# Performance work log

Hardware: AMD Instinct MI355X
Metric: run time of the kernel (lower is better)

The kernel has to match this reference:

```python
import jax, jax.numpy as jnp
import numpy as np

B, C, H, W = 1, 256, 48, 64
HW = H * W
HIDDEN, CTX = 128, 64
LEVELS, RADIUS = 4, 4
WIN = 2 * RADIUS + 1
P = WIN * WIN                     # 81 lookup points per level
CORR_DIM = P * LEVELS             # 324
TOP_K = 3
ITERS = 4
STEP_ROT, STEP_TRANS = 0.02, 0.02


def _sample_templates():
    # 12 directions x 3 scales + identity = 37 pose perturbations (as in __init__)
    base = [([0,0,0],[1,0,0]),([0,0,0],[-1,0,0]),([0,0,0],[0,1,0]),([0,0,0],[0,-1,0]),
            ([0,0,0],[0,0,1]),([0,0,0],[0,0,-1]),([1,0,0],[0,0,0]),([-1,0,0],[0,0,0]),
            ([0,1,0],[0,0,0]),([0,-1,0],[0,0,0]),([0,0,1],[0,0,0]),([0,0,-1],[0,0,0])]
    scales = np.array([0.25, 1.0, 4.0], np.float32)
    rot = np.repeat(np.array([r for r, _ in base], np.float32), 3, axis=0)
    trs = np.repeat(np.array([t for _, t in base], np.float32), 3, axis=0)
    sc = np.tile(scales, 12)
    axes = rot / np.clip(np.linalg.norm(rot, axis=1, keepdims=True), 1e-8, None)
    ha = STEP_ROT * sc / 2.0
    dq = np.stack([np.cos(ha), axes[:, 0]*np.sin(ha), axes[:, 1]*np.sin(ha), axes[:, 2]*np.sin(ha)], -1)
    dt = trs * (STEP_TRANS * sc[:, None])
    dq = np.concatenate([dq, [[1., 0., 0., 0.]]], 0)
    dt = np.concatenate([dt, [[0., 0., 0.]]], 0)
    return jnp.asarray(dq), jnp.asarray(dt)

DQ, DT = _sample_templates()     # (37,4), (37,3)
N_SAMPLES = DQ.shape[0]


def qmul(q, r):
    w1, x1, y1, z1 = jnp.moveaxis(q, -1, 0)
    w2, x2, y2, z2 = jnp.moveaxis(r, -1, 0)
    return jnp.stack([w1*w2 - x1*x2 - y1*y2 - z1*z2,
                      w1*x2 + x1*w2 + y1*z2 - z1*y2,
                      w1*y2 - x1*z2 + y1*w2 + z1*x2,
                      w1*z2 + x1*y2 - y1*x2 + z1*w2], -1)


def qapply(q, v):
    qv = jnp.concatenate([jnp.zeros(v.shape[:-1] + (1,), v.dtype), v], -1)
    qc = q * jnp.array([1., -1., -1., -1.], q.dtype)
    return qmul(qmul(q, qv), qc)[..., 1:]


def quat_to_R(q):
    w, x, y, z = jnp.moveaxis(q, -1, 0)
    R = jnp.stack([1-2*(y*y+z*z), 2*(x*y-w*z), 2*(x*z+w*y),
                   2*(x*y+w*z), 1-2*(x*x+z*z), 2*(y*z-w*x),
                   2*(x*z-w*y), 2*(y*z+w*x), 1-2*(x*x+y*y)], -1)
    return R.reshape(q.shape[:-1] + (3, 3))


def conv3(x, w, b):
    y = jax.lax.conv_general_dilated(x, w, (1, 1), 'SAME',
                                     dimension_numbers=('NCHW', 'OIHW', 'NCHW'))
    return y + b[None, :, None, None]


def bilinear_lookup(corr_flat, Hl, Wl, x, y):
    # corr_flat: (B,HW,Hl*Wl); x,y: (B,N,HW,P) -> (B,N,HW,P), zero padding outside
    x0 = jnp.floor(x)
    y0 = jnp.floor(y)
    out = jnp.zeros(x.shape, corr_flat.dtype)
    def gather(idx):
        g = lambda ix: jnp.take_along_axis(corr_flat, ix, axis=-1)
        return jax.vmap(g, in_axes=1, out_axes=1)(idx)   # vmap over N, no corr copy
    for dx_, dy_ in ((0, 0), (1, 0), (0, 1), (1, 1)):
        xi = x0 + dx_
        yi = y0 + dy_
        wgt = (1 - jnp.abs(x - xi)) * (1 - jnp.abs(y - yi))
        valid = (xi >= 0) & (xi < Wl) & (yi >= 0) & (yi < Hl)
        idx = (jnp.clip(yi, 0, Hl - 1) * Wl + jnp.clip(xi, 0, Wl - 1)).astype(jnp.int32)
        out = out + jnp.where(valid, wgt, 0.0) * gather(idx)
    return out


def _forward(fmap_rgb, fmap_depth, depth, context, intrinsics,
             Wz, bz, Wr, br, Wq, bq, Wh, bh, Wfc, bfc):
    f32 = jnp.float32
    fx = 60. + 40. * intrinsics[:, 0]
    fy = 60. + 40. * intrinsics[:, 1]
    cx = W / 2. + 4. * (intrinsics[:, 2] - 0.5)
    cy = H / 2. + 4. * (intrinsics[:, 3] - 0.5)
    d = 4.0 + 20.0 * depth                                  # (B,H,W) metric depth

    # 4D correlation pyramid: corr[b,i,:,:] = <fmap_depth pixel i, fmap_rgb>
    fd = fmap_depth.reshape(B, C, HW).transpose(0, 2, 1)    # (B,HW,C)
    corr = jnp.einsum('bic,bchw->bihw', fd, fmap_rgb) / jnp.sqrt(f32(C))
    pyramid = []
    cl, Hl, Wl = corr, H, W
    for _ in range(LEVELS):
        pyramid.append((cl.reshape(B, HW, Hl * Wl), Hl, Wl))
        cl = cl.reshape(B, HW, Hl // 2, 2, Wl // 2, 2).mean(axis=(3, 5))
        Hl //= 2
        Wl //= 2

    # back-projected depth points (B,HW,3)
    vv, uu = jnp.meshgrid(jnp.arange(H, dtype=f32), jnp.arange(W, dtype=f32), indexing='ij')
    uu = uu.reshape(HW)
    vv = vv.reshape(HW)
    df = d.reshape(B, HW)
    X = jnp.stack([(uu[None] - cx[:, None]) / fx[:, None] * df,
                   (vv[None] - cy[:, None]) / fy[:, None] * df, df], -1)

    off = jnp.arange(-RADIUS, RADIUS + 1, dtype=f32)
    oy, ox = jnp.meshgrid(off, off, indexing='ij')
    ox = ox.reshape(P)
    oy = oy.reshape(P)

    pose = jnp.tile(jnp.array([1., 0., 0., 0., 0., 0., 0.], f32)[None, :], (B, 1))
    h = jnp.zeros((B, HIDDEN, H, W), f32)

    for _ in range(ITERS):
        qc, tc = pose[:, :4], pose[:, 4:7]
        quats = qmul(qc[:, None, :], DQ[None])              # (B,N,4)
        quats = quats / jnp.linalg.norm(quats, axis=-1, keepdims=True)
        trans = tc[:, None, :] + qapply(qc[:, None, :], DT[None])
        Rm = quat_to_R(quats)                               # (B,N,3,3)
        Xc = jnp.einsum('bnij,bpj->bnpi', Rm, X) + trans[:, :, None, :]
        z = jnp.clip(Xc[..., 2], 0.1, None)
        u = fx[:, None, None] * Xc[..., 0] / z + cx[:, None, None]   # (B,N,HW)
        v = fy[:, None, None] * Xc[..., 1] / z + cy[:, None, None]
        feats = []
        for lvl, (cfl, Hl_, Wl_) in enumerate(pyramid):
            s = f32(2 ** lvl)
            xl = u[..., None] / s + ox
            yl = v[..., None] / s + oy
            feats.append(bilinear_lookup(cfl, Hl_, Wl_, xl, yl))
        cf = jnp.concatenate(feats, -1)                     # (B,N,HW,CORR_DIM)
        conf = cf.mean(axis=(2, 3))                         # (B,N) sample confidence
        topv, topi = jax.lax.top_k(conf, TOP_K)
        wk = jax.nn.softmax(topv, axis=-1)                  # confidence-weighted top-K
        idx = jnp.broadcast_to(topi[:, :, None, None], (B, TOP_K, HW, CORR_DIM))
        sel = jnp.take_along_axis(cf, idx, axis=1)
        fused = (wk[:, :, None, None] * sel).sum(1)         # (B,HW,CORR_DIM)
        fused = fused.transpose(0, 2, 1).reshape(B, CORR_DIM, H, W)

        # ConvGRU update
        x_in = jnp.concatenate([fused, context], 1)
        hx = jnp.concatenate([h, x_in], 1)
        zg = jax.nn.sigmoid(conv3(hx, Wz, bz))
        rg = jax.nn.sigmoid(conv3(hx, Wr, br))
        qg = jnp.tanh(conv3(jnp.concatenate([rg * h, x_in], 1), Wq, bq))
        h = (1 - zg) * h + zg * qg

        # 7D pose delta head + quaternion/Lie-style update
        feat = jax.nn.relu(conv3(h, Wh, bh)).mean(axis=(2, 3))
        delta = 0.01 * (feat @ Wfc + bfc)                   # (B,7)
        dq = jnp.concatenate([1.0 + delta[:, :1], delta[:, 1:4]], -1)
        dq = dq / jnp.linalg.norm(dq, axis=-1, keepdims=True)
        tn = tc + qapply(qc, delta[:, 4:7])
        qn = qmul(qc, dq)
        qn = qn / jnp.linalg.norm(qn, axis=-1, keepdims=True)
        pose = jnp.concatenate([qn, tn], -1)
    return pose


def setup_inputs() -> dict:
    key = jax.random.key(0)
    ks = jax.random.split(key, 12)
    rn = lambda k, shape, s=1.0: s * jax.random.normal(k, shape, jnp.float32)
    Gin = HIDDEN + CORR_DIM + CTX
    sc = 1.0 / np.sqrt(Gin * 9)
    sh = 1.0 / np.sqrt(HIDDEN * 9)
    return {
        'fmap_rgb': rn(ks[0], (B, C, H, W)),
        'fmap_depth': rn(ks[1], (B, C, H, W)),
        'depth': jax.random.uniform(ks[2], (B, H, W), jnp.float32),
        'context': rn(ks[3], (B, CTX, H, W)),
        'intrinsics': jax.random.uniform(ks[4], (B, 4), jnp.float32),
        'Wz': rn(ks[5], (HIDDEN, Gin, 3, 3), sc), 'bz': jnp.zeros((HIDDEN,), jnp.float32),
        'Wr': rn(ks[6], (HIDDEN, Gin, 3, 3), sc), 'br': jnp.zeros((HIDDEN,), jnp.float32),
        'Wq': rn(ks[7], (HIDDEN, Gin, 3, 3), sc), 'bq': jnp.zeros((HIDDEN,), jnp.float32),
        'Wh': rn(ks[8], (HIDDEN, HIDDEN, 3, 3), sh), 'bh': jnp.zeros((HIDDEN,), jnp.float32),
        'Wfc': rn(ks[9], (HIDDEN, 7), 1.0 / np.sqrt(HIDDEN)), 'bfc': jnp.zeros((7,), jnp.float32),
    }


def reference(fmap_rgb, fmap_depth, depth, context, intrinsics,
              Wz, bz, Wr, br, Wq, bq, Wh, bh, Wfc, bfc):
    return _forward(fmap_rgb, fmap_depth, depth, context, intrinsics,
                    Wz, bz, Wr, br, Wq, bq, Wh, bh, Wfc, bfc)
```

## Files before the change

kernel.cpp:

```cpp
#include <hip/hip_runtime.h>
#include <math.h>

constexpr int kH = 48, kW = 64, kHW = 3072, kC = 256;
constexpr int kHidden = 128, kCtx = 64;
constexpr int kP = 81, kCorrDim = 324;
constexpr int kNS = 37, kIters = 4;
constexpr int kGin = kHidden + kCorrDim + kCtx;
constexpr int kCinPad = 544;
constexpr int kStepsBig = 17 * 9;
constexpr int kStepsH = 4 * 9;

constexpr int kSB0 = 0, kSB1 = 4292, kSB2 = 5720, kSB3 = 6292, kSBTot = 6580;
constexpr int kHB0 = 0, kHB1 = 3552, kHB2 = 4560, kHB3 = 4872, kHBTot = 4980;

constexpr size_t U_CORR0 = 0;
constexpr size_t U_CORR1 = U_CORR0 + (size_t)kHW * 3072;
constexpr size_t U_CORR2 = U_CORR1 + (size_t)kHW * 768;
constexpr size_t U_CORR3 = U_CORR2 + (size_t)kHW * 192;
constexpr size_t U_END0  = U_CORR3 + (size_t)kHW * 48;
constexpr size_t F_X     = U_END0 / 2;
constexpr size_t F_H     = F_X + (size_t)kHW * 3;
constexpr size_t F_ZPRE  = F_H + (size_t)kHidden * kHW;
constexpr size_t F_END1  = F_ZPRE + (size_t)kHidden * kHW;
constexpr size_t U_BUFT  = F_END1 * 2;
constexpr size_t U_RHT   = U_BUFT + (size_t)kHW * kCinPad;
constexpr size_t U_PZR   = U_RHT + (size_t)kHW * kHidden;
constexpr size_t U_PQ    = U_PZR + (size_t)kStepsBig * 256 * 32;
constexpr size_t U_PH    = U_PQ + (size_t)kStepsBig * 128 * 32;
constexpr size_t U_END2  = U_PH + (size_t)kStepsH * 128 * 32;
constexpr size_t F_BZR   = (U_END2 + 2) / 2;
constexpr size_t F_CONF  = F_BZR + 256;
constexpr size_t F_TK    = F_CONF + 64;
constexpr size_t F_POSE  = F_TK + 16;
constexpr size_t F_FEAT  = F_POSE + 16;
constexpr size_t F_END3  = F_FEAT + 128;
constexpr size_t U_FDT   = F_END3 * 2;
constexpr size_t U_QT    = U_FDT + (size_t)kHW * kC;
constexpr size_t U_SBOX  = U_FDT;

typedef __attribute__((ext_vector_type(8))) short short8;
typedef __attribute__((ext_vector_type(4))) float f32x4;

__device__ inline unsigned short f2b(float f) {
  unsigned int u = __float_as_uint(f);
  unsigned int r = u + 0x7FFF + ((u >> 16) & 1);
  return (unsigned short)(r >> 16);
}
__device__ inline float b2f(unsigned short u) {
  return __uint_as_float(((unsigned int)u) << 16);
}
__device__ inline int clampi(int v, int lo, int hi) { return min(max(v, lo), hi); }

__constant__ float c_rot[12][3] = {
  {0,0,0},{0,0,0},{0,0,0},{0,0,0},{0,0,0},{0,0,0},
  {1,0,0},{-1,0,0},{0,1,0},{0,-1,0},{0,0,1},{0,0,-1}};
__constant__ float c_trs[12][3] = {
  {1,0,0},{-1,0,0},{0,1,0},{0,-1,0},{0,0,1},{0,0,-1},
  {0,0,0},{0,0,0},{0,0,0},{0,0,0},{0,0,0},{0,0,0}};

__device__ inline void d_qmul(const float* q, const float* r, float* o) {
  o[0] = q[0]*r[0] - q[1]*r[1] - q[2]*r[2] - q[3]*r[3];
  o[1] = q[0]*r[1] + q[1]*r[0] + q[2]*r[3] - q[3]*r[2];
  o[2] = q[0]*r[2] - q[1]*r[3] + q[2]*r[0] + q[3]*r[1];
  o[3] = q[0]*r[3] + q[1]*r[2] - q[2]*r[1] + q[3]*r[0];
}
__device__ inline void d_qapply(const float* q, const float* v, float* o) {
// ... 28 lines not shown
    float ha = 0.02f * sc * 0.5f;
    float sh = sinf(ha), ch = cosf(ha);
    dq[0] = ch; dq[1] = ax * sh; dq[2] = ay * sh; dq[3] = az * sh;
    dt[0] = c_trs[j][0] * (0.02f * sc);
    dt[1] = c_trs[j][1] * (0.02f * sc);
    dt[2] = c_trs[j][2] * (0.02f * sc);
  }
  float qn[4];
  d_qmul(qc, dq, qn);
  float inv = 1.f / sqrtf(qn[0]*qn[0] + qn[1]*qn[1] + qn[2]*qn[2] + qn[3]*qn[3]);
  qn[0] *= inv; qn[1] *= inv; qn[2] *= inv; qn[3] *= inv;
  float tr[3];
  d_qapply(qc, dt, tr);
  float w = qn[0], x = qn[1], y = qn[2], z = qn[3];
  S[0] = 1.f - 2.f*(y*y + z*z); S[1] = 2.f*(x*y - w*z);       S[2] = 2.f*(x*z + w*y);
  S[3] = 2.f*(x*y + w*z);       S[4] = 1.f - 2.f*(x*x + z*z); S[5] = 2.f*(y*z - w*x);
  S[6] = 2.f*(x*z - w*y);       S[7] = 2.f*(y*z + w*x);       S[8] = 1.f - 2.f*(x*x + y*y);
  S[9]  = tc[0] + tr[0];
  S[10] = tc[1] + tr[1];
  S[11] = tc[2] + tr[2];
}
__device__ inline void project_uv(const float* S, const float* Xp, const float* intr,
                                  float& u, float& v) {
  float xc0 = S[0]*Xp[0] + S[1]*Xp[1] + S[2]*Xp[2] + S[9];
  float xc1 = S[3]*Xp[0] + S[4]*Xp[1] + S[5]*Xp[2] + S[10];
  float xc2 = S[6]*Xp[0] + S[7]*Xp[1] + S[8]*Xp[2] + S[11];
  float z = fmaxf(xc2, 0.1f);
  float fx, fy, cx, cy;
  d_intr(intr, fx, fy, cx, cy);
  u = fx * xc0 / z + cx;
  v = fy * xc1 / z + cy;
}

__global__ void init_k(const float* __restrict__ ctx, const float* __restrict__ bz,
                       const float* __restrict__ br, const float* __restrict__ depth,
                       const float* __restrict__ intr, float* __restrict__ h,
                       unsigned short* __restrict__ bufT, float* __restrict__ bzr,
                       float* __restrict__ X, float* __restrict__ conf,
                       float* __restrict__ feat, float* __restrict__ pose) {
  int idx = blockIdx.x * blockDim.x + threadIdx.x;
  if (idx < kHidden * kHW) {
    h[idx] = 0.f;
    int p = idx >> 7, c = idx & 127;
    bufT[(size_t)p * kCinPad + c] = 0;
  }
  if (idx < kHW * 92) {
    int p = idx / 92, c = idx % 92;
    unsigned short v = 0;
    if (c < 64) v = f2b(ctx[(size_t)c * kHW + p]);
    bufT[(size_t)p * kCinPad + 452 + c] = v;
  }
  if (idx < kHW) {
    float fx, fy, cx, cy;
    d_intr(intr, fx, fy, cx, cy);
    float d = 4.f + 20.f * depth[idx];
    float u = (float)(idx % kW), v = (float)(idx / kW);
    X[idx*3+0] = (u - cx) / fx * d;
    X[idx*3+1] = (v - cy) / fy * d;
    X[idx*3+2] = d;
  }
  if (idx < 256) bzr[idx] = (idx < 128) ? bz[idx] : br[idx - 128];
  if (idx < 64) conf[idx] = 0.f;
  if (idx < 128) feat[idx] = 0.f;
  if (idx == 0) {
    pose[0] = 1.f;
    for (int j = 1; j < 7; ++j) pose[j] = 0.f;
  }
}

__global__ void pack_k(const float* __restrict__ W0, const float* __restrict__ W1,
                       int ocSplit, int OC, int nsteps, int nchunks, int Cin,
                       unsigned short* __restrict__ P) {
  int idx = blockIdx.x * blockDim.x + threadIdx.x;
  int total = nsteps * OC * 4;
  if (idx >= total) return;
  int g = idx & 3;
  int oc = (idx >> 2) % OC;
  int s = idx / (OC * 4);
  int tap = s / nchunks, cc = s % nchunks;
  union { unsigned short u[8]; uint4 q; } v;
#pragma unroll
  for (int j = 0; j < 8; ++j) {
    int ci = cc * 32 + g * 8 + j;
    float w = 0.f;
    if (ci < Cin)
      w = (oc < ocSplit) ? W0[((size_t)oc * Cin + ci) * 9 + tap]
                         : W1[((size_t)(oc - ocSplit) * Cin + ci) * 9 + tap];
    v.u[j] = f2b(w);
  }
  *(uint4*)&P[(size_t)idx * 8] = v.q;
}

__global__ __launch_bounds__(256) void t_bf16_k(const float* __restrict__ src,
                                                unsigned short* __restrict__ dst) {
  __shared__ float t[64][65];
  const int tid = threadIdx.x;
  const int p0 = blockIdx.x * 64, c0 = blockIdx.y * 64;
  const int tx = tid & 63, ty = tid >> 6;
  for (int cl = ty; cl < 64; cl += 4)
    t[cl][tx] = src[(size_t)(c0 + cl) * kHW + p0 + tx];
  __syncthreads();
  for (int pl = ty; pl < 64; pl += 4)
    dst[(size_t)(p0 + pl) * kC + c0 + tx] = f2b(t[tx][pl]);
}

__global__ __launch_bounds__(256) void corr_mfma_k(const unsigned short* __restrict__ fdT,
                                                   const unsigned short* __restrict__ qT,
                                                   unsigned short* __restrict__ Cg) {
  const int tid = threadIdx.x;
  const int wv = tid >> 6, lane = tid & 63;
  const int m = lane & 15, kg = lane >> 4;
  const int i0 = blockIdx.y * 128 + wv * 32;
// ... 69 lines not shown
  const int i = blockIdx.x;
  const int tid = threadIdx.x;
  const int wv = tid >> 6, lane = tid & 63;

  for (int idx = tid; idx < 4080; idx += 256) {
    float v;
    if (idx < 3072)      v = b2f(corr0[(size_t)i * 3072 + idx]);
    else if (idx < 3840) v = b2f(corr1[(size_t)i * 768 + idx - 3072]);
    else if (idx < 4032) v = b2f(corr2[(size_t)i * 192 + idx - 3840]);
    else                 v = b2f(corr3[(size_t)i * 48 + idx - 4032]);
    pyr[idx] = v;
  }
  __syncthreads();

  const int lvl_off[4] = {0, 3072, 3840, 4032};
  for (int r = wv; r < 90; r += 4) {
    int lvl, y;
    if (r < 48)      { lvl = 0; y = r; }
    else if (r < 72) { lvl = 1; y = r - 48; }
    else if (r < 84) { lvl = 2; y = r - 72; }
    else             { lvl = 3; y = r - 84; }
    const int Wl = kW >> lvl;
    float* row = &pyr[lvl_off[lvl] + y * Wl];
    float v = (lane < Wl) ? row[lane] : 0.f;
#pragma unroll
    for (int o = 1; o < 64; o <<= 1) {
      float tv = __shfl_up(v, o, 64);
      if (lane >= o) v += tv;
    }
    if (lane < Wl) row[lane] = v;
  }
  __syncthreads();

  for (int c = tid; c < kHBTot; c += 256) {
    int lvl, rem;
    if (c < kHB1)      { lvl = 0; rem = c; }
    else if (c < kHB2) { lvl = 1; rem = c - kHB1; }
    else if (c < kHB3) { lvl = 2; rem = c - kHB2; }
    else               { lvl = 3; rem = c - kHB3; }
    const int Wl = kW >> lvl, Wp = Wl + 10;
    const int y = rem / Wp, as = rem % Wp;
    const float* pref = &pyr[lvl_off[lvl] + y * Wl];
    float Hv = 0.f;
    if (as >= 1) Hv = pref[min(Wl - 1, as - 1)];
    if (as >= 10) Hv -= pref[as - 10];
    hb[c] = Hv;
  }
  __syncthreads();

  const int hoff[4] = {kHB0, kHB1, kHB2, kHB3};
  if (tid < 160) {
    if (tid < 74)       colpref<48>(hb + kHB0 + tid, 74);
    else if (tid < 116) colpref<24>(hb + kHB1 + (tid - 74), 42);
    else if (tid < 142) colpref<12>(hb + kHB2 + (tid - 116), 26);
    else                colpref<6>(hb + kHB3 + (tid - 142), 18);
  }
  __syncthreads();

  unsigned short* out = Sbox + (size_t)i * kSBTot;
  for (int c = tid; c < kSBTot; c += 256) {
    int lvl, rem;
    if (c < kSB1)      { lvl = 0; rem = c; }
    else if (c < kSB2) { lvl = 1; rem = c - kSB1; }
    else if (c < kSB3) { lvl = 2; rem = c - kSB2; }
    else               { lvl = 3; rem = c - kSB3; }
    const int Wl = kW >> lvl, Hl = kH >> lvl, Wp = Wl + 10;
    const int bp = rem / Wp, as = rem % Wp;
    const float* col = &hb[hoff[lvl] + as];
    float S = 0.f;
    if (bp >= 1) S = col[(size_t)min(Hl - 1, bp - 1) * Wp];
    if (bp >= 10) S -= col[(size_t)(bp - 10) * Wp];
    out[c] = f2b(S);
  }
}

__global__ __launch_bounds__(256) void conf_k(const unsigned short* __restrict__ Sbox,
                                              const float* __restrict__ X,
                                              const float* __restrict__ pose,
                                              const float* __restrict__ intr,
                                              float* __restrict__ conf) {
  const int idx = blockIdx.x * 256 + threadIdx.x;
  const int n = idx / kHW, i = idx - n * kHW;
  float S[12];
  sample_Rt(n, pose, S);
  float Xp[3] = {X[i*3], X[i*3+1], X[i*3+2]};
  float u, v;
  project_uv(S, Xp, intr, u, v);
  const unsigned short* sb = Sbox + (size_t)i * kSBTot;
  float tot = 0.f;
#pragma unroll
  for (int l = 0; l < 4; ++l) {
    const int Wp = (kW >> l) + 10, Hp = (kH >> l) + 10;
    const int so = (l == 0) ? kSB0 : (l == 1) ? kSB1 : (l == 2) ? kSB2 : kSB3;
    const float s = (float)(1 << l);
    const float bx = u / s, by = v / s;
    const float fbx = floorf(bx), fby = floorf(by);
    const int x0 = (int)fbx, y0 = (int)fby;
    const float fx = bx - fbx, fy = by - fby;
    const int xa = clampi(x0 + 5, 0, Wp - 1), xb = clampi(x0 + 6, 0, Wp - 1);
    const int ya = clampi(y0 + 5, 0, Hp - 1), yb = clampi(y0 + 6, 0, Hp - 1);
    const float s00 = b2f(sb[so + ya * Wp + xa]), s10 = b2f(sb[so + ya * Wp + xb]);
    const float s01 = b2f(sb[so + yb * Wp + xa]), s11 = b2f(sb[so + yb * Wp + xb]);
    tot += (1.f - fx) * (1.f - fy) * s00 + fx * (1.f - fy) * s10 +
           (1.f - fx) * fy * s01 + fx * fy * s11;
  }
#pragma unroll
  for (int o = 32; o; o >>= 1) tot += __shfl_xor(tot, o, 64);
  if ((threadIdx.x & 63) == 0) atomicAdd(&conf[n], tot);
}

__global__ void topk_k(float* __restrict__ conf, float* __restrict__ tkw,
                       int* __restrict__ tki) {
  if (threadIdx.x != 0) return;
  const float scale = 1.f / ((float)kHW * (float)kCorrDim);
  float c[kNS];
  for (int n = 0; n < kNS; ++n) c[n] = conf[n] * scale;
  int id[3] = {-1, -1, -1};
  float v[3];
  for (int k = 0; k < 3; ++k) {
    float best = -1e30f;
    int bi = -1;
    for (int n = 0; n < kNS; ++n) {
      if (n == id[0] || n == id[1] || n == id[2]) continue;
      if (c[n] > best) { best = c[n]; bi = n; }
    }
    v[k] = best;
    id[k] = bi;
  }
  float m = v[0];
  float e0 = expf(v[0] - m), e1 = expf(v[1] - m), e2 = expf(v[2] - m);
  float s = e0 + e1 + e2;
  tkw[0] = e0 / s; tkw[1] = e1 / s; tkw[2] = e2 / s;
  tki[0] = id[0]; tki[1] = id[1]; tki[2] = id[2];
  for (int n = 0; n < kNS; ++n) conf[n] = 0.f;
}

__global__ __launch_bounds__(256) void fused_k(const unsigned short* __restrict__ corr0,
                                               const unsigned short* __restrict__ corr1,
                                               const unsigned short* __restrict__ corr2,
                                               const unsigned short* __restrict__ corr3,
                                               const float* __restrict__ X,
                                               const float* __restrict__ pose,
                                               const float* __restrict__ intr,
                                               const float* __restrict__ tkw,
                                               const int* __restrict__ tki,
                                               unsigned short* __restrict__ bufT) {
  __shared__ float win[12][10][12];
  __shared__ float s_fx[12], s_fy[12];
  __shared__ int   s_ix[12], s_iy[12];
  __shared__ float s_w[3];
  const int i = blockIdx.x;
  const int tid = threadIdx.x;

  if (tid < 3) {
    int n = tki[tid];
    s_w[tid] = tkw[tid];
    float S[12];
    sample_Rt(n, pose, S);
    float Xp[3] = {X[i*3], X[i*3+1], X[i*3+2]};
    float u, v;
    project_uv(S, Xp, intr, u, v);
#pragma unroll
    for (int l = 0; l < 4; ++l) {
      float s = (float)(1 << l);
      float bx = u / s, by = v / s;
      float fbx = floorf(bx), fby = floorf(by);
      s_ix[tid*4 + l] = (int)fbx;
      s_iy[tid*4 + l] = (int)fby;
      s_fx[tid*4 + l] = bx - fbx;
      s_fy[tid*4 + l] = by - fby;
    }
  }
  __syncthreads();

  for (int sidx = tid; sidx < 1200; sidx += 256) {
    const int w = sidx / 100, rem = sidx % 100;
    const int rr = rem / 10, cc = rem % 10;
    const int lvl = w & 3;
    const int Wl = kW >> lvl, Hl = kH >> lvl;
    const unsigned short* base =
        (lvl == 0) ? corr0 : (lvl == 1) ? corr1 : (lvl == 2) ? corr2 : corr3;
    const int y = s_iy[w] - 4 + rr;
    const int x = s_ix[w] - 4 + cc;
    float v = 0.f;
    if (y >= 0 && y < Hl && x >= 0 && x < Wl)
      v = b2f(base[(size_t)i * (Hl * Wl) + y * Wl + x]);
    win[w][rr][cc] = v;
  }
  __syncthreads();

  for (int d = tid; d < kCorrDim; d += 256) {
    const int lvl = d / kP;
    const int o = d % kP;
    const int oyi = o / 9, oxi = o % 9;
    float val = 0.f;
#pragma unroll
    for (int k = 0; k < 3; ++k) {
      const int w = k * 4 + lvl;
      const float fx = s_fx[w], fy = s_fy[w];
      const float w00 = (1.f - fx) * (1.f - fy), w10 = fx * (1.f - fy);
      const float w01 = (1.f - fx) * fy, w11 = fx * fy;
      val += s_w[k] * (w00 * win[w][oyi][oxi] + w10 * win[w][oyi][oxi + 1] +
                       w01 * win[w][oyi + 1][oxi] + w11 * win[w][oyi + 1][oxi + 1]);
    }
    bufT[(size_t)i * kCinPad + kHidden + d] = f2b(val);
  }
}

template<int OC, int NCH, bool QMODE>
__device__ inline void conv_kloop(const unsigned short* __restrict__ inT,
                                  const unsigned short* __restrict__ rhT,
                                  const unsigned short* __restrict__ P,
                                  int y, int xbase, int wv, int lane, int ocBlock,
                                  f32x4 (&acc)[2]) {
  const int m = lane & 15, kg = lane >> 4;
  const int ocW = ocBlock + wv * 16;
#pragma unroll
  for (int tap = 0; tap < 9; ++tap) {
    const int dy = tap / 3 - 1, dx = tap % 3 - 1;
    const int yy = y + dy;
    if (yy < 0 || yy >= kH) continue;
    const int xs0 = xbase + m + dx, xs1 = xbase + 16 + m + dx;
    const bool v0 = (xs0 >= 0) && (xs0 < kW);
    const bool v1 = (xs1 >= 0) && (xs1 < kW);
    const int px0 = yy * kW + xs0, px1 = yy * kW + xs1;
    const unsigned short* a_base = P + ((size_t)(tap * NCH) * OC + ocW + m) * 32 + kg * 8;
#pragma unroll
    for (int cc = 0; cc < NCH; ++cc) {
      const unsigned short* srcB;
      int stride;
      if (QMODE && cc < 4) { srcB = rhT; stride = kHidden; }
      else                 { srcB = inT; stride = kCinPad; }
      short8 a0 = *(const short8*)(a_base + (size_t)cc * OC * 32);
      short8 b0 = {0, 0, 0, 0, 0, 0, 0, 0};
      short8 b1 = {0, 0, 0, 0, 0, 0, 0, 0};
      if (v0) b0 = *(const short8*)(srcB + (size_t)px0 * stride + cc * 32 + kg * 8);
      if (v1) b1 = *(const short8*)(srcB + (size_t)px1 * stride + cc * 32 + kg * 8);
      acc[0] = __builtin_amdgcn_mfma_f32_16x16x32_bf16(a0, b0, acc[0], 0, 0, 0);
      acc[1] = __builtin_amdgcn_mfma_f32_16x16x32_bf16(a0, b1, acc[1], 0, 0, 0);
    }
  }
}

__global__ __launch_bounds__(256) void conv_zr_k(const unsigned short* __restrict__ bufT,
                                                 const unsigned short* __restrict__ P,
                                                 const float* __restrict__ bzr,
                                                 float* __restrict__ zpre,
                                                 const float* __restrict__ hbuf,
                                                 unsigned short* __restrict__ rhT) {
  const int tid = threadIdx.x;
  const int wv = tid >> 6, lane = tid & 63;
  const int y = blockIdx.y >> 1, xbase = (blockIdx.y & 1) * 32;
  const int ocBlock = blockIdx.x * 64;
  f32x4 acc[2] = {{0.f,0.f,0.f,0.f},{0.f,0.f,0.f,0.f}};
  conv_kloop<256, 17, false>(bufT, nullptr, P, y, xbase, wv, lane, ocBlock, acc);
  const int m = lane & 15, kg = lane >> 4;
  const int ocW = ocBlock + wv * 16;
#pragma unroll
  for (int t = 0; t < 2; ++t)
#pragma unroll
    for (int r = 0; r < 4; ++r) {
      const int oc = ocW + kg * 4 + r;
      const int px = y * kW + xbase + t * 16 + m;
      const float val = acc[t][r] + bzr[oc];
      if (oc < kHidden) {
        zpre[(size_t)oc * kHW + px] = val;
      } else {
        const float rg = 1.f / (1.f + expf(-val));
        rhT[(size_t)px * kHidden + oc - kHidden] = f2b(rg * hbuf[(size_t)(oc - kHidden) * kHW + px]);
      }
    }
}

__global__ __launch_bounds__(256) void conv_q_k(unsigned short* __restrict__ bufT,
                                                const unsigned short* __restrict__ rhT,
                                                const unsigned short* __restrict__ P,
                                                const float* __restrict__ bq,
                                                const float* __restrict__ zpre,
                                                float* __restrict__ hbuf) {
  const int tid = threadIdx.x;
  const int wv = tid >> 6, lane = tid & 63;
  const int y = blockIdx.y >> 1, xbase = (blockIdx.y & 1) * 32;
  const int ocBlock = blockIdx.x * 64;
  f32x4 acc[2] = {{0.f,0.f,0.f,0.f},{0.f,0.f,0.f,0.f}};
  conv_kloop<128, 17, true>(bufT, rhT, P, y, xbase, wv, lane, ocBlock, acc);
  const int m = lane & 15, kg = lane >> 4;
  const int ocW = ocBlock + wv * 16;
#pragma unroll
  for (int t = 0; t < 2; ++t)
#pragma unroll
    for (int r = 0; r < 4; ++r) {
      const int oc = ocW + kg * 4 + r;
      const int px = y * kW + xbase + t * 16 + m;
      const size_t off = (size_t)oc * kHW + px;
      const float q = acc[t][r] + bq[oc];
      const float zg = 1.f / (1.f + expf(-zpre[off]));
      const float hn = (1.f - zg) * hbuf[off] + zg * tanhf(q);
      hbuf[off] = hn;
      bufT[(size_t)px * kCinPad + oc] = f2b(hn);
    }
}

__global__ __launch_bounds__(256) void conv_h_k(const unsigned short* __restrict__ bufT,
                                                const unsigned short* __restrict__ P,
                                                const float* __restrict__ bh,
                                                float* __restrict__ feat) {
  const int tid = threadIdx.x;
  const int wv = tid >> 6, lane = tid & 63;
  const int y = blockIdx.y >> 1, xbase = (blockIdx.y & 1) * 32;
  const int ocBlock = blockIdx.x * 64;
  f32x4 acc[2] = {{0.f,0.f,0.f,0.f},{0.f,0.f,0.f,0.f}};
  conv_kloop<128, 4, false>(bufT, nullptr, P, y, xbase, wv, lane, ocBlock, acc);
  const int m = lane & 15, kg = lane >> 4;
  const int ocW = ocBlock + wv * 16;
#pragma unroll
  for (int r = 0; r < 4; ++r) {
    const int oc = ocW + kg * 4 + r;
    const float bv = bh[oc];
    float v = fmaxf(acc[0][r] + bv, 0.f) + fmaxf(acc[1][r] + bv, 0.f);
    v += __shfl_xor(v, 1, 64);
    v += __shfl_xor(v, 2, 64);
    v += __shfl_xor(v, 4, 64);
    v += __shfl_xor(v, 8, 64);
    if (m == 0) atomicAdd(&feat[oc], v);
  }
}

__global__ void pose_update_k(float* __restrict__ feat, const float* __restrict__ Wfc,
                              const float* __restrict__ bfc, float* __restrict__ pose,
                              float* __restrict__ out) {
  __shared__ float s_d[7];
  int t = threadIdx.x;
  if (t < 7) {
    float s = 0.f;
    const float inv = 1.f / (float)kHW;
    for (int k = 0; k < kHidden; ++k) s += (feat[k] * inv) * Wfc[k * 7 + t];
    s_d[t] = 0.01f * (s + bfc[t]);
  }
  __syncthreads();
  if (t < kHidden) feat[t] = 0.f;
  if (t != 0) return;
  float qc[4] = {pose[0], pose[1], pose[2], pose[3]};
  float tc[3] = {pose[4], pose[5], pose[6]};
  float dq[4] = {1.f + s_d[0], s_d[1], s_d[2], s_d[3]};
  float inv = 1.f / sqrtf(dq[0]*dq[0] + dq[1]*dq[1] + dq[2]*dq[2] + dq[3]*dq[3]);
  dq[0] *= inv; dq[1] *= inv; dq[2] *= inv; dq[3] *= inv;
  float dv[3] = {s_d[4], s_d[5], s_d[6]};
  float rv[3];
  d_qapply(qc, dv, rv);
  float tn[3] = {tc[0] + rv[0], tc[1] + rv[1], tc[2] + rv[2]};
  float qn[4];
  d_qmul(qc, dq, qn);
  float inv2 = 1.f / sqrtf(qn[0]*qn[0] + qn[1]*qn[1] + qn[2]*qn[2] + qn[3]*qn[3]);
  qn[0] *= inv2; qn[1] *= inv2; qn[2] *= inv2; qn[3] *= inv2;
  pose[0] = qn[0]; pose[1] = qn[1]; pose[2] = qn[2]; pose[3] = qn[3];
  pose[4] = tn[0]; pose[5] = tn[1]; pose[6] = tn[2];
  out[0] = qn[0]; out[1] = qn[1]; out[2] = qn[2]; out[3] = qn[3];
  out[4] = tn[0]; out[5] = tn[1]; out[6] = tn[2];
}

extern "C" void kernel_launch(void* const* d_in, const int* in_sizes, int n_in,
                              void* d_out, int out_size, void* d_ws, size_t ws_size,
                              hipStream_t stream) {
  const float* frgb  = (const float*)d_in[0];
  const float* fdep  = (const float*)d_in[1];
  const float* depth = (const float*)d_in[2];
  const float* ctx   = (const float*)d_in[3];
  const float* intr  = (const float*)d_in[4];
  const float* Wz = (const float*)d_in[5];
  const float* bz = (const float*)d_in[6];
  const float* Wr = (const float*)d_in[7];
  const float* br = (const float*)d_in[8];
  const float* Wq = (const float*)d_in[9];
  const float* bq = (const float*)d_in[10];
  const float* Wh = (const float*)d_in[11];
  const float* bh = (const float*)d_in[12];
  const float* Wfc = (const float*)d_in[13];
  const float* bfc = (const float*)d_in[14];
  float* outp = (float*)d_out;

  float* ws = (float*)d_ws;
  unsigned short* us = (unsigned short*)d_ws;
  unsigned short* corr0 = us + U_CORR0;
  unsigned short* corr1 = us + U_CORR1;
  unsigned short* corr2 = us + U_CORR2;
  unsigned short* corr3 = us + U_CORR3;
  float* X    = ws + F_X;
  float* hbuf = ws + F_H;
  float* zpre = ws + F_ZPRE;
  unsigned short* bufT = us + U_BUFT;
  unsigned short* rhT  = us + U_RHT;
  unsigned short* Pzr  = us + U_PZR;
  unsigned short* Pq   = us + U_PQ;
  unsigned short* Ph   = us + U_PH;
  float* bzr  = ws + F_BZR;
  float* conf = ws + F_CONF;
  float* tkw  = ws + F_TK;
  int*   tki  = (int*)(ws + F_TK + 3);
  float* pose = ws + F_POSE;
  float* feat = ws + F_FEAT;
  unsigned short* fdT  = us + U_FDT;
  unsigned short* qT   = us + U_QT;
  unsigned short* Sbox = us + U_SBOX;

  init_k<<<1536, 256, 0, stream>>>(ctx, bz, br, depth, intr, hbuf, bufT, bzr, X,
                                   conf, feat, pose);
  pack_k<<<(kStepsBig * 256 * 4 + 255) / 256, 256, 0, stream>>>(Wz, Wr, 128, 256,
                                                                kStepsBig, 17, kGin, Pzr);
  pack_k<<<(kStepsBig * 128 * 4 + 255) / 256, 256, 0, stream>>>(Wq, Wq, 128, 128,
                                                                kStepsBig, 17, kGin, Pq);
  pack_k<<<(kStepsH * 128 * 4 + 255) / 256, 256, 0, stream>>>(Wh, Wh, 128, 128,
                                                              kStepsH, 4, kHidden, Ph);
  t_bf16_k<<<dim3(48, 4), 256, 0, stream>>>(fdep, fdT);
  t_bf16_k<<<dim3(48, 4), 256, 0, stream>>>(frgb, qT);
  corr_mfma_k<<<dim3(24, 24), 256, 0, stream>>>(fdT, qT, corr0);
  {
    int t1 = kHW * 24 * 32, t2 = kHW * 12 * 16, t3 = kHW * 6 * 8;
    pool2_k<<<(t1 + 255) / 256, 256, 0, stream>>>(corr0, corr1, 48, 64);
    pool2_k<<<(t2 + 255) / 256, 256, 0, stream>>>(corr1, corr2, 24, 32);
    pool2_k<<<(t3 + 255) / 256, 256, 0, stream>>>(corr2, corr3, 12, 16);
  }
  boxbuild_k<<<kHW, 256, 0, stream>>>(corr0, corr1, corr2, corr3, Sbox);

  for (int it = 0; it < kIters; ++it) {
    conf_k<<<444, 256, 0, stream>>>(Sbox, X, pose, intr, conf);
    topk_k<<<1, 64, 0, stream>>>(conf, tkw, tki);
    fused_k<<<kHW, 256, 0, stream>>>(corr0, corr1, corr2, corr3, X, pose, intr,
                                     tkw, tki, bufT);
    conv_zr_k<<<dim3(4, 96), 256, 0, stream>>>(bufT, Pzr, bzr, zpre, hbuf, rhT);
    conv_q_k<<<dim3(2, 96), 256, 0, stream>>>(bufT, rhT, Pq, bq, zpre, hbuf);
    conv_h_k<<<dim3(2, 96), 256, 0, stream>>>(bufT, Ph, bh, feat);
    pose_update_k<<<1, 128, 0, stream>>>(feat, Wfc, bfc, pose, outp);
  }
}
```

Before: 909.8 us.

## Use zero-padded activation buffers and tile-contiguous weight packing; fold topk into fused kernel

Activations for the GRU convolutions now live in spatially zero-padded (50x66) bf16 buffers, split into hidden, r*h and corr/context parts. This removes the per-tap bounds checks and the masked loads in the MFMA conv loop. Weights are repacked so each 16-output tile's data is contiguous per step. The single-thread topk kernel is removed: every fused_k block recomputes top-3 from conf, and conf is reset in pose_update instead. The boxbuild level loops are also unrolled per level with constant widths. The trade-offs are redundant topk work in every block and extra memory for the padded buffers.

```diff
diff --git a/kernel.cpp b/kernel.cpp
--- a/kernel.cpp
+++ b/kernel.cpp
@@ -6,9 +6,9 @@
 constexpr int kP = 81, kCorrDim = 324;
 constexpr int kNS = 37, kIters = 4;
 constexpr int kGin = kHidden + kCorrDim + kCtx;
-constexpr int kCinPad = 544;
-constexpr int kStepsBig = 17 * 9;
-constexpr int kStepsH = 4 * 9;
+constexpr int kWp2 = 66, kHp2 = 50, kPix = 3300;
+constexpr int kCF = 416;
+constexpr int kCHh = 128;
 
 constexpr int kSB0 = 0, kSB1 = 4292, kSB2 = 5720, kSB3 = 6292, kSBTot = 6580;
 constexpr int kHB0 = 0, kHB1 = 3552, kHB2 = 4560, kHB3 = 4872, kHBTot = 4980;
@@ -22,16 +22,16 @@
 constexpr size_t F_H     = F_X + (size_t)kHW * 3;
 constexpr size_t F_ZPRE  = F_H + (size_t)kHidden * kHW;
 constexpr size_t F_END1  = F_ZPRE + (size_t)kHidden * kHW;
-constexpr size_t U_BUFT  = F_END1 * 2;
-constexpr size_t U_RHT   = U_BUFT + (size_t)kHW * kCinPad;
-constexpr size_t U_PZR   = U_RHT + (size_t)kHW * kHidden;
-constexpr size_t U_PQ    = U_PZR + (size_t)kStepsBig * 256 * 32;
-constexpr size_t U_PH    = U_PQ + (size_t)kStepsBig * 128 * 32;
-constexpr size_t U_END2  = U_PH + (size_t)kStepsH * 128 * 32;
-constexpr size_t F_BZR   = (U_END2 + 2) / 2;
+constexpr size_t U_FCT   = F_END1 * 2;
+constexpr size_t U_HT    = U_FCT + (size_t)kPix * kCF;
+constexpr size_t U_RHT   = U_HT + (size_t)kPix * kCHh;
+constexpr size_t U_PZR   = U_RHT + (size_t)kPix * kCHh;
+constexpr size_t U_PQ    = U_PZR + (size_t)16 * 9 * 17 * 512;
+constexpr size_t U_PH    = U_PQ + (size_t)8 * 9 * 17 * 512;
+constexpr size_t U_END2  = U_PH + (size_t)8 * 9 * 4 * 512;
+constexpr size_t F_BZR   = U_END2 / 2 + 1;
 constexpr size_t F_CONF  = F_BZR + 256;
-constexpr size_t F_TK    = F_CONF + 64;
-constexpr size_t F_POSE  = F_TK + 16;
+constexpr size_t F_POSE  = F_CONF + 64;
 constexpr size_t F_FEAT  = F_POSE + 16;
 constexpr size_t F_END3  = F_FEAT + 128;
 constexpr size_t U_FDT   = F_END3 * 2;
@@ -126,23 +126,32 @@
   v = fy * xc1 / z + cy;
 }
 
-__global__ void init_k(const float* __restrict__ ctx, const float* __restrict__ bz,
-                       const float* __restrict__ br, const float* __restrict__ depth,
-                       const float* __restrict__ intr, float* __restrict__ h,
-                       unsigned short* __restrict__ bufT, float* __restrict__ bzr,
-                       float* __restrict__ X, float* __restrict__ conf,
-                       float* __restrict__ feat, float* __restrict__ pose) {
+__global__ void init_k(float* __restrict__ h, unsigned int* __restrict__ zbase,
+                       float* __restrict__ conf, float* __restrict__ feat,
+                       float* __restrict__ pose) {
+  const size_t nz = ((size_t)kPix * (kCF + 2 * kCHh)) / 2;
+  for (size_t i = blockIdx.x * blockDim.x + threadIdx.x; i < nz;
+       i += (size_t)gridDim.x * blockDim.x)
+    zbase[i] = 0;
   int idx = blockIdx.x * blockDim.x + threadIdx.x;
-  if (idx < kHidden * kHW) {
-    h[idx] = 0.f;
-    int p = idx >> 7, c = idx & 127;
-    bufT[(size_t)p * kCinPad + c] = 0;
-  }
-  if (idx < kHW * 92) {
-    int p = idx / 92, c = idx % 92;
-    unsigned short v = 0;
-    if (c < 64) v = f2b(ctx[(size_t)c * kHW + p]);
-    bufT[(size_t)p * kCinPad + 452 + c] = v;
+  if (idx < kHidden * kHW) h[idx] = 0.f;
+  if (idx < 64) conf[idx] = 0.f;
+  if (idx < 128) feat[idx] = 0.f;
+  if (idx == 0) {
+    pose[0] = 1.f;
+    for (int j = 1; j < 7; ++j) pose[j] = 0.f;
+  }
+}
+
+__global__ void init2_k(const float* __restrict__ ctx, const float* __restrict__ bz,
+                        const float* __restrict__ br, const float* __restrict__ depth,
+                        const float* __restrict__ intr, unsigned short* __restrict__ fcT,
+                        float* __restrict__ bzr, float* __restrict__ X) {
+  int idx = blockIdx.x * blockDim.x + threadIdx.x;
+  if (idx < kHW * 64) {
+    int p = idx >> 6, c = idx & 63;
+    int ppix = ((p >> 6) + 1) * kWp2 + (p & 63) + 1;
+    fcT[(size_t)ppix * kCF + kCorrDim + c] = f2b(ctx[(size_t)c * kHW + p]);
   }
   if (idx < kHW) {
     float fx, fy, cx, cy;
@@ -154,24 +163,22 @@
     X[idx*3+2] = d;
   }
   if (idx < 256) bzr[idx] = (idx < 128) ? bz[idx] : br[idx - 128];
-  if (idx < 64) conf[idx] = 0.f;
-  if (idx < 128) feat[idx] = 0.f;
-  if (idx == 0) {
-    pose[0] = 1.f;
-    for (int j = 1; j < 7; ++j) pose[j] = 0.f;
-  }
 }
 
 __global__ void pack_k(const float* __restrict__ W0, const float* __restrict__ W1,
-                       int ocSplit, int OC, int nsteps, int nchunks, int Cin,
+                       int ocSplit, int OC, int NCH, int Cin,
                        unsigned short* __restrict__ P) {
   int idx = blockIdx.x * blockDim.x + threadIdx.x;
-  int total = nsteps * OC * 4;
+  int total = (OC / 16) * 9 * NCH * 64;
   if (idx >= total) return;
   int g = idx & 3;
-  int oc = (idx >> 2) % OC;
-  int s = idx / (OC * 4);
-  int tap = s / nchunks, cc = s % nchunks;
+  int m = (idx >> 2) & 15;
+  int rest = idx >> 6;
+  int cc = rest % NCH;
+  int rest2 = rest / NCH;
+  int tap = rest2 % 9;
+  int ot = rest2 / 9;
+  int oc = ot * 16 + m;
   union { unsigned short u[8]; uint4 q; } v;
 #pragma unroll
   for (int j = 0; j < 8; ++j) {
@@ -307,23 +314,40 @@
   }
   __syncthreads();
 
-  for (int c = tid; c < kHBTot; c += 256) {
-    int lvl, rem;
-    if (c < kHB1)      { lvl = 0; rem = c; }
-    else if (c < kHB2) { lvl = 1; rem = c - kHB1; }
-    else if (c < kHB3) { lvl = 2; rem = c - kHB2; }
-    else               { lvl = 3; rem = c - kHB3; }
-    const int Wl = kW >> lvl, Wp = Wl + 10;
-    const int y = rem / Wp, as = rem % Wp;
-    const float* pref = &pyr[lvl_off[lvl] + y * Wl];
+  for (int c = tid; c < 3552; c += 256) {
+    int y = c / 74, as = c % 74;
+    const float* pref = &pyr[y * 64];
     float Hv = 0.f;
-    if (as >= 1) Hv = pref[min(Wl - 1, as - 1)];
+    if (as >= 1) Hv = pref[min(63, as - 1)];
     if (as >= 10) Hv -= pref[as - 10];
-    hb[c] = Hv;
-  }
-  __syncthreads();
-
-  const int hoff[4] = {kHB0, kHB1, kHB2, kHB3};
+    hb[kHB0 + c] = Hv;
+  }
+  for (int c = tid; c < 1008; c += 256) {
+    int y = c / 42, as = c % 42;
+    const float* pref = &pyr[3072 + y * 32];
+    float Hv = 0.f;
+    if (as >= 1) Hv = pref[min(31, as - 1)];
+    if (as >= 10) Hv -= pref[as - 10];
+    hb[kHB1 + c] = Hv;
+  }
+  for (int c = tid; c < 312; c += 256) {
+    int y = c / 26, as = c % 26;
+    const float* pref = &pyr[3840 + y * 16];
+    float Hv = 0.f;
+    if (as >= 1) Hv = pref[min(15, as - 1)];
+    if (as >= 10) Hv -= pref[as - 10];
+    hb[kHB2 + c] = Hv;
+  }
+  for (int c = tid; c < 108; c += 256) {
+    int y = c / 18, as = c % 18;
+    const float* pref = &pyr[4032 + y * 8];
+    float Hv = 0.f;
+    if (as >= 1) Hv = pref[min(7, as - 1)];
+    if (as >= 10) Hv -= pref[as - 10];
+    hb[kHB3 + c] = Hv;
+  }
+  __syncthreads();
+
   if (tid < 160) {
     if (tid < 74)       colpref<48>(hb + kHB0 + tid, 74);
     else if (tid < 116) colpref<24>(hb + kHB1 + (tid - 74), 42);
@@ -333,19 +357,37 @@
   __syncthreads();
 
   unsigned short* out = Sbox + (size_t)i * kSBTot;
-  for (int c = tid; c < kSBTot; c += 256) {
-    int lvl, rem;
-    if (c < kSB1)      { lvl = 0; rem = c; }
-    else if (c < kSB2) { lvl = 1; rem = c - kSB1; }
-    else if (c < kSB3) { lvl = 2; rem = c - kSB2; }
-    else               { lvl = 3; rem = c - kSB3; }
-    const int Wl = kW >> lvl, Hl = kH >> lvl, Wp = Wl + 10;
-    const int bp = rem / Wp, as = rem % Wp;
-    const float* col = &hb[hoff[lvl] + as];
+  for (int c = tid; c < 4292; c += 256) {
+    int bp = c / 74, as = c % 74;
+    const float* col = &hb[kHB0 + as];
     float S = 0.f;
-    if (bp >= 1) S = col[(size_t)min(Hl - 1, bp - 1) * Wp];
-    if (bp >= 10) S -= col[(size_t)(bp - 10) * Wp];
-    out[c] = f2b(S);
+    if (bp >= 1) S = col[min(47, bp - 1) * 74];
+    if (bp >= 10) S -= col[(bp - 10) * 74];
+    out[kSB0 + c] = f2b(S);
+  }
+  for (int c = tid; c < 1428; c += 256) {
+    int bp = c / 42, as = c % 42;
+    const float* col = &hb[kHB1 + as];
+    float S = 0.f;
+    if (bp >= 1) S = col[min(23, bp - 1) * 42];
+    if (bp >= 10) S -= col[(bp - 10) * 42];
+    out[kSB1 + c] = f2b(S);
+  }
+  for (int c = tid; c < 572; c += 256) {
+    int bp = c / 26, as = c % 26;
+    const float* col = &hb[kHB2 + as];
+    float S = 0.f;
+    if (bp >= 1) S = col[min(11, bp - 1) * 26];
+    if (bp >= 10) S -= col[(bp - 10) * 26];
+    out[kSB2 + c] = f2b(S);
+  }
+  for (int c = tid; c < 288; c += 256) {
+    int bp = c / 18, as = c % 18;
+    const float* col = &hb[kHB3 + as];
+    float S = 0.f;
+    if (bp >= 1) S = col[min(5, bp - 1) * 18];
+    if (bp >= 10) S -= col[(bp - 10) * 18];
+    out[kSB3 + c] = f2b(S);
   }
 }
 
@@ -384,32 +426,6 @@
   if ((threadIdx.x & 63) == 0) atomicAdd(&conf[n], tot);
 }
 
-__global__ void topk_k(float* __restrict__ conf, float* __restrict__ tkw,
-                       int* __restrict__ tki) {
-  if (threadIdx.x != 0) return;
-  const float scale = 1.f / ((float)kHW * (float)kCorrDim);
-  float c[kNS];
-  for (int n = 0; n < kNS; ++n) c[n] = conf[n] * scale;
-  int id[3] = {-1, -1, -1};
-  float v[3];
-  for (int k = 0; k < 3; ++k) {
-    float best = -1e30f;
-    int bi = -1;
-    for (int n = 0; n < kNS; ++n) {
-      if (n == id[0] || n == id[1] || n == id[2]) continue;
-      if (c[n] > best) { best = c[n]; bi = n; }
-    }
-    v[k] = best;
-    id[k] = bi;
-  }
-  float m = v[0];
-  float e0 = expf(v[0] - m), e1 = expf(v[1] - m), e2 = expf(v[2] - m);
-  float s = e0 + e1 + e2;
-  tkw[0] = e0 / s; tkw[1] = e1 / s; tkw[2] = e2 / s;
-  tki[0] = id[0]; tki[1] = id[1]; tki[2] = id[2];
-  for (int n = 0; n < kNS; ++n) conf[n] = 0.f;
-}
-
 __global__ __launch_bounds__(256) void fused_k(const unsigned short* __restrict__ corr0,
                                                const unsigned short* __restrict__ corr1,
                                                const unsigned short* __restrict__ corr2,
@@ -417,19 +433,42 @@
                                                const float* __restrict__ X,
                                                const float* __restrict__ pose,
                                                const float* __restrict__ intr,
-                                               const float* __restrict__ tkw,
-                                               const int* __restrict__ tki,
-                                               unsigned short* __restrict__ bufT) {
+                                               const float* __restrict__ conf,
+                                               unsigned short* __restrict__ fcT) {
   __shared__ float win[12][10][12];
   __shared__ float s_fx[12], s_fy[12];
   __shared__ int   s_ix[12], s_iy[12];
   __shared__ float s_w[3];
+  __shared__ int   s_id[3];
   const int i = blockIdx.x;
   const int tid = threadIdx.x;
 
+  if (tid == 0) {
+    const float scale = 1.f / ((float)kHW * (float)kCorrDim);
+    float c[kNS];
+    for (int n = 0; n < kNS; ++n) c[n] = conf[n] * scale;
+    int id[3] = {-1, -1, -1};
+    float v[3];
+    for (int k = 0; k < 3; ++k) {
+      float best = -1e30f;
+      int bi = -1;
+      for (int n = 0; n < kNS; ++n) {
+        if (n == id[0] || n == id[1] || n == id[2]) continue;
+        if (c[n] > best) { best = c[n]; bi = n; }
+      }
+      v[k] = best;
+      id[k] = bi;
+    }
+    float m = v[0];
+    float e0 = expf(v[0] - m), e1 = expf(v[1] - m), e2 = expf(v[2] - m);
+    float s = e0 + e1 + e2;
+    s_w[0] = e0 / s; s_w[1] = e1 / s; s_w[2] = e2 / s;
+    s_id[0] = id[0]; s_id[1] = id[1]; s_id[2] = id[2];
+  }
+  __syncthreads();
+
   if (tid < 3) {
-    int n = tki[tid];
-    s_w[tid] = tkw[tid];
+    int n = s_id[tid];
     float S[12];
     sample_Rt(n, pose, S);
     float Xp[3] = {X[i*3], X[i*3+1], X[i*3+2]};
@@ -464,6 +503,7 @@
   }
   __syncthreads();
 
+  const int ppix = ((i >> 6) + 1) * kWp2 + (i & 63) + 1;
   for (int d = tid; d < kCorrDim; d += 256) {
     const int lvl = d / kP;
     const int o = d % kP;
@@ -478,46 +518,46 @@
       val += s_w[k] * (w00 * win[w][oyi][oxi] + w10 * win[w][oyi][oxi + 1] +
                        w01 * win[w][oyi + 1][oxi] + w11 * win[w][oyi + 1][oxi + 1]);
     }
-    bufT[(size_t)i * kCinPad + kHidden + d] = f2b(val);
-  }
-}
-
-template<int OC, int NCH, bool QMODE>
-__device__ inline void conv_kloop(const unsigned short* __restrict__ inT,
-                                  const unsigned short* __restrict__ rhT,
-                                  const unsigned short* __restrict__ P,
-                                  int y, int xbase, int wv, int lane, int ocBlock,
+    fcT[(size_t)ppix * kCF + d] = f2b(val);
+  }
+}
+
+template<int NCHH, int NCHF>
+__device__ inline void conv_core2(const unsigned short* __restrict__ srcH,
+                                  const unsigned short* __restrict__ srcF,
+                                  const unsigned short* __restrict__ A,
+                                  int y, int xbase, int ot, int lane,
                                   f32x4 (&acc)[2]) {
   const int m = lane & 15, kg = lane >> 4;
-  const int ocW = ocBlock + wv * 16;
+  constexpr int NCH = NCHH + NCHF;
+  const unsigned short* a_base = A + (size_t)ot * (9 * NCH * 512) + m * 32 + kg * 8;
+  const int pix0 = (y + 1) * kWp2 + (xbase + 1) + m;
 #pragma unroll
   for (int tap = 0; tap < 9; ++tap) {
     const int dy = tap / 3 - 1, dx = tap % 3 - 1;
-    const int yy = y + dy;
-    if (yy < 0 || yy >= kH) continue;
-    const int xs0 = xbase + m + dx, xs1 = xbase + 16 + m + dx;
-    const bool v0 = (xs0 >= 0) && (xs0 < kW);
-    const bool v1 = (xs1 >= 0) && (xs1 < kW);
-    const int px0 = yy * kW + xs0, px1 = yy * kW + xs1;
-    const unsigned short* a_base = P + ((size_t)(tap * NCH) * OC + ocW + m) * 32 + kg * 8;
+    const int po = pix0 + dy * kWp2 + dx;
+    const unsigned short* bh0 = srcH + (size_t)po * kCHh + kg * 8;
+    const unsigned short* bf0 = srcF + (size_t)po * kCF + kg * 8;
 #pragma unroll
     for (int cc = 0; cc < NCH; ++cc) {
-      const unsigned short* srcB;
-      int stride;
-      if (QMODE && cc < 4) { srcB = rhT; stride = kHidden; }
-      else                 { srcB = inT; stride = kCinPad; }
-      short8 a0 = *(const short8*)(a_base + (size_t)cc * OC * 32);
-      short8 b0 = {0, 0, 0, 0, 0, 0, 0, 0};
-      short8 b1 = {0, 0, 0, 0, 0, 0, 0, 0};
-      if (v0) b0 = *(const short8*)(srcB + (size_t)px0 * stride + cc * 32 + kg * 8);
-      if (v1) b1 = *(const short8*)(srcB + (size_t)px1 * stride + cc * 32 + kg * 8);
-      acc[0] = __builtin_amdgcn_mfma_f32_16x16x32_bf16(a0, b0, acc[0], 0, 0, 0);
-      acc[1] = __builtin_amdgcn_mfma_f32_16x16x32_bf16(a0, b1, acc[1], 0, 0, 0);
+      const int s = tap * NCH + cc;
+      short8 a = *(const short8*)(a_base + (size_t)s * 512);
+      short8 b0, b1;
+      if (cc < NCHH) {
+        b0 = *(const short8*)(bh0 + cc * 32);
+        b1 = *(const short8*)(bh0 + 16 * kCHh + cc * 32);
+      } else {
+        b0 = *(const short8*)(bf0 + (cc - NCHH) * 32);
+        b1 = *(const short8*)(bf0 + 16 * kCF + (cc - NCHH) * 32);
+      }
+      acc[0] = __builtin_amdgcn_mfma_f32_16x16x32_bf16(a, b0, acc[0], 0, 0, 0);
+      acc[1] = __builtin_amdgcn_mfma_f32_16x16x32_bf16(a, b1, acc[1], 0, 0, 0);
     }
   }
 }
 
-__global__ __launch_bounds__(256) void conv_zr_k(const unsigned short* __restrict__ bufT,
+__global__ __launch_bounds__(256) void conv_zr_k(const unsigned short* __restrict__ hT,
+                                                 const unsigned short* __restrict__ fcT,
                                                  const unsigned short* __restrict__ P,
                                                  const float* __restrict__ bzr,
                                                  float* __restrict__ zpre,
@@ -526,29 +566,32 @@
   const int tid = threadIdx.x;
   const int wv = tid >> 6, lane = tid & 63;
   const int y = blockIdx.y >> 1, xbase = (blockIdx.y & 1) * 32;
-  const int ocBlock = blockIdx.x * 64;
+  const int ot = blockIdx.x * 4 + wv;
   f32x4 acc[2] = {{0.f,0.f,0.f,0.f},{0.f,0.f,0.f,0.f}};
-  conv_kloop<256, 17, false>(bufT, nullptr, P, y, xbase, wv, lane, ocBlock, acc);
+  conv_core2<4, 13>(hT, fcT, P, y, xbase, ot, lane, acc);
   const int m = lane & 15, kg = lane >> 4;
-  const int ocW = ocBlock + wv * 16;
 #pragma unroll
   for (int t = 0; t < 2; ++t)
 #pragma unroll
     for (int r = 0; r < 4; ++r) {
-      const int oc = ocW + kg * 4 + r;
-      const int px = y * kW + xbase + t * 16 + m;
+      const int oc = ot * 16 + kg * 4 + r;
+      const int pxx = xbase + t * 16 + m;
+      const int px = y * kW + pxx;
       const float val = acc[t][r] + bzr[oc];
       if (oc < kHidden) {
         zpre[(size_t)oc * kHW + px] = val;
       } else {
         const float rg = 1.f / (1.f + expf(-val));
-        rhT[(size_t)px * kHidden + oc - kHidden] = f2b(rg * hbuf[(size_t)(oc - kHidden) * kHW + px]);
+        const int ppix = (y + 1) * kWp2 + pxx + 1;
+        rhT[(size_t)ppix * kCHh + oc - kHidden] =
+            f2b(rg * hbuf[(size_t)(oc - kHidden) * kHW + px]);
       }
     }
 }
 
-__global__ __launch_bounds__(256) void conv_q_k(unsigned short* __restrict__ bufT,
-                                                const unsigned short* __restrict__ rhT,
+__global__ __launch_bounds__(256) void conv_q_k(const unsigned short* __restrict__ rhT,
+                                                const unsigned short* __restrict__ fcT,
+                                                unsigned short* __restrict__ hT,
                                                 const unsigned short* __restrict__ P,
                                                 const float* __restrict__ bq,
                                                 const float* __restrict__ zpre,
@@ -556,41 +599,41 @@
   const int tid = threadIdx.x;
   const int wv = tid >> 6, lane = tid & 63;
   const int y = blockIdx.y >> 1, xbase = (blockIdx.y & 1) * 32;
-  const int ocBlock = blockIdx.x * 64;
+  const int ot = blockIdx.x * 4 + wv;
   f32x4 acc[2] = {{0.f,0.f,0.f,0.f},{0.f,0.f,0.f,0.f}};
-  conv_kloop<128, 17, true>(bufT, rhT, P, y, xbase, wv, lane, ocBlock, acc);
+  conv_core2<4, 13>(rhT, fcT, P, y, xbase, ot, lane, acc);
   const int m = lane & 15, kg = lane >> 4;
-  const int ocW = ocBlock + wv * 16;
 #pragma unroll
   for (int t = 0; t < 2; ++t)
 #pragma unroll
     for (int r = 0; r < 4; ++r) {
-      const int oc = ocW + kg * 4 + r;
-      const int px = y * kW + xbase + t * 16 + m;
+      const int oc = ot * 16 + kg * 4 + r;
+      const int pxx = xbase + t * 16 + m;
+      const int px = y * kW + pxx;
       const size_t off = (size_t)oc * kHW + px;
       const float q = acc[t][r] + bq[oc];
       const float zg = 1.f / (1.f + expf(-zpre[off]));
       const float hn = (1.f - zg) * hbuf[off] + zg * tanhf(q);
       hbuf[off] = hn;
-      bufT[(size_t)px * kCinPad + oc] = f2b(hn);
+      const int ppix = (y + 1) * kWp2 + pxx + 1;
+      hT[(size_t)ppix * kCHh + oc] = f2b(hn);
     }
 }
 
-__global__ __launch_bounds__(256) void conv_h_k(const unsigned short* __restrict__ bufT,
+__global__ __launch_bounds__(256) void conv_h_k(const unsigned short* __restrict__ hT,
                                                 const unsigned short* __restrict__ P,
                                                 const float* __restrict__ bh,
                                                 float* __restrict__ feat) {
   const int tid = threadIdx.x;
   const int wv = tid >> 6, lane = tid & 63;
   const int y = blockIdx.y >> 1, xbase = (blockIdx.y & 1) * 32;
-  const int ocBlock = blockIdx.x * 64;
+  const int ot = blockIdx.x * 4 + wv;
   f32x4 acc[2] = {{0.f,0.f,0.f,0.f},{0.f,0.f,0.f,0.f}};
-  conv_kloop<128, 4, false>(bufT, nullptr, P, y, xbase, wv, lane, ocBlock, acc);
+  conv_core2<4, 0>(hT, hT, P, y, xbase, ot, lane, acc);
   const int m = lane & 15, kg = lane >> 4;
-  const int ocW = ocBlock + wv * 16;
 #pragma unroll
   for (int r = 0; r < 4; ++r) {
-    const int oc = ocW + kg * 4 + r;
+    const int oc = ot * 16 + kg * 4 + r;
     const float bv = bh[oc];
     float v = fmaxf(acc[0][r] + bv, 0.f) + fmaxf(acc[1][r] + bv, 0.f);
     v += __shfl_xor(v, 1, 64);
@@ -601,7 +644,8 @@
   }
 }
 
-__global__ void pose_update_k(float* __restrict__ feat, const float* __restrict__ Wfc,
+__global__ void pose_update_k(float* __restrict__ feat, float* __restrict__ conf,
+                              const float* __restrict__ Wfc,
                               const float* __restrict__ bfc, float* __restrict__ pose,
                               float* __restrict__ out) {
   __shared__ float s_d[7];
@@ -614,6 +658,7 @@
   }
   __syncthreads();
   if (t < kHidden) feat[t] = 0.f;
+  if (t < 64) conf[t] = 0.f;
   if (t != 0) return;
   float qc[4] = {pose[0], pose[1], pose[2], pose[3]};
   float tc[3] = {pose[4], pose[5], pose[6]};
@@ -663,29 +708,28 @@
   float* X    = ws + F_X;
   float* hbuf = ws + F_H;
   float* zpre = ws + F_ZPRE;
-  unsigned short* bufT = us + U_BUFT;
-  unsigned short* rhT  = us + U_RHT;
-  unsigned short* Pzr  = us + U_PZR;
-  unsigned short* Pq   = us + U_PQ;
-  unsigned short* Ph   = us + U_PH;
+  unsigned short* fcT = us + U_FCT;
+  unsigned short* hT  = us + U_HT;
+  unsigned short* rhT = us + U_RHT;
+  unsigned short* Pzr = us + U_PZR;
+  unsigned short* Pq  = us + U_PQ;
+  unsigned short* Ph  = us + U_PH;
   float* bzr  = ws + F_BZR;
   float* conf = ws + F_CONF;
-  float* tkw  = ws + F_TK;
-  int*   tki  = (int*)(ws + F_TK + 3);
   float* pose = ws + F_POSE;
   float* feat = ws + F_FEAT;
   unsigned short* fdT  = us + U_FDT;
   unsigned short* qT   = us + U_QT;
   unsigned short* Sbox = us + U_SBOX;
 
-  init_k<<<1536, 256, 0, stream>>>(ctx, bz, br, depth, intr, hbuf, bufT, bzr, X,
-                                   conf, feat, pose);
-  pack_k<<<(kStepsBig * 256 * 4 + 255) / 256, 256, 0, stream>>>(Wz, Wr, 128, 256,
-                                                                kStepsBig, 17, kGin, Pzr);
-  pack_k<<<(kStepsBig * 128 * 4 + 255) / 256, 256, 0, stream>>>(Wq, Wq, 128, 128,
-                                                                kStepsBig, 17, kGin, Pq);
-  pack_k<<<(kStepsH * 128 * 4 + 255) / 256, 256, 0, stream>>>(Wh, Wh, 128, 128,
-                                                              kStepsH, 4, kHidden, Ph);
+  init_k<<<1536, 256, 0, stream>>>(hbuf, (unsigned int*)fcT, conf, feat, pose);
+  init2_k<<<768, 256, 0, stream>>>(ctx, bz, br, depth, intr, fcT, bzr, X);
+  pack_k<<<(16 * 9 * 17 * 64 + 255) / 256, 256, 0, stream>>>(Wz, Wr, 128, 256, 17,
+                                                             kGin, Pzr);
+  pack_k<<<(8 * 9 * 17 * 64 + 255) / 256, 256, 0, stream>>>(Wq, Wq, 128, 128, 17,
+                                                            kGin, Pq);
+  pack_k<<<(8 * 9 * 4 * 64 + 255) / 256, 256, 0, stream>>>(Wh, Wh, 128, 128, 4,
+                                                           kHidden, Ph);
   t_bf16_k<<<dim3(48, 4), 256, 0, stream>>>(fdep, fdT);
   t_bf16_k<<<dim3(48, 4), 256, 0, stream>>>(frgb, qT);
   corr_mfma_k<<<dim3(24, 24), 256, 0, stream>>>(fdT, qT, corr0);
@@ -699,12 +743,11 @@
 
   for (int it = 0; it < kIters; ++it) {
     conf_k<<<444, 256, 0, stream>>>(Sbox, X, pose, intr, conf);
-    topk_k<<<1, 64, 0, stream>>>(conf, tkw, tki);
     fused_k<<<kHW, 256, 0, stream>>>(corr0, corr1, corr2, corr3, X, pose, intr,
-                                     tkw, tki, bufT);
-    conv_zr_k<<<dim3(4, 96), 256, 0, stream>>>(bufT, Pzr, bzr, zpre, hbuf, rhT);
-    conv_q_k<<<dim3(2, 96), 256, 0, stream>>>(bufT, rhT, Pq, bq, zpre, hbuf);
-    conv_h_k<<<dim3(2, 96), 256, 0, stream>>>(bufT, Ph, bh, feat);
-    pose_update_k<<<1, 128, 0, stream>>>(feat, Wfc, bfc, pose, outp);
-  }
-}
+                                     conf, fcT);
+    conv_zr_k<<<dim3(4, 96), 256, 0, stream>>>(hT, fcT, Pzr, bzr, zpre, hbuf, rhT);
+    conv_q_k<<<dim3(2, 96), 256, 0, stream>>>(rhT, fcT, hT, Pq, bq, zpre, hbuf);
+    conv_h_k<<<dim3(2, 96), 256, 0, stream>>>(hT, Ph, bh, feat);
+    pose_update_k<<<1, 128, 0, stream>>>(feat, conf, Wfc, bfc, pose, outp);
+  }
+}
```

Measured after the change: 875.5 us. 3.8% less time.
